# Optimization experiments

Hardware: AMD Instinct MI355X
Metric: run time of the kernel (lower is better)

The kernel has to match this reference:

```python
import math
import jax, jax.numpy as jnp
import numpy as np

N_NODES = 10000
N_EDGES = 160000
F_IN = 256
HID = 500
N_OUT = 100


def setup_inputs() -> dict:
    key = jax.random.key(0)
    ks = jax.random.split(key, 20)
    inp = {}
    inp['x'] = jax.random.normal(ks[0], (N_NODES, F_IN), jnp.float32)
    inp['edge_src'] = jax.random.randint(ks[1], (N_EDGES,), 0, N_NODES, jnp.int32)
    inp['edge_dst'] = jax.random.randint(ks[2], (N_EDGES,), 0, N_NODES, jnp.int32)
    inp['edge_weight'] = jax.random.uniform(ks[3], (N_EDGES,), jnp.float32)
    s1 = 1.0 / math.sqrt(F_IN)
    s2 = 1.0 / math.sqrt(HID)
    inp['W1_rel'] = jax.random.uniform(ks[4], (HID, F_IN), jnp.float32, -s1, s1)
    inp['b1'] = jax.random.uniform(ks[5], (HID,), jnp.float32, -s1, s1)
    inp['W1_root'] = jax.random.uniform(ks[6], (HID, F_IN), jnp.float32, -s1, s1)
    inp['p1_w'] = jax.random.uniform(ks[7], (HID,), jnp.float32, -s2, s2)
    inp['W2_rel'] = jax.random.uniform(ks[8], (HID, HID), jnp.float32, -s2, s2)
    inp['b2'] = jax.random.uniform(ks[9], (HID,), jnp.float32, -s2, s2)
    inp['W2_root'] = jax.random.uniform(ks[10], (HID, HID), jnp.float32, -s2, s2)
    inp['p2_w'] = jax.random.uniform(ks[11], (HID,), jnp.float32, -s2, s2)
    s3 = 1.0 / math.sqrt(1000)
    inp['lin1_W'] = jax.random.uniform(ks[12], (2000, 1000), jnp.float32, -s3, s3)
    inp['lin1_b'] = jax.random.uniform(ks[13], (2000,), jnp.float32, -s3, s3)
    s4 = 1.0 / math.sqrt(2000)
    inp['lin2_W'] = jax.random.uniform(ks[14], (4000, 2000), jnp.float32, -s4, s4)
    inp['lin2_b'] = jax.random.uniform(ks[15], (4000,), jnp.float32, -s4, s4)
    s5 = 1.0 / math.sqrt(4000)
    inp['lin3_W'] = jax.random.uniform(ks[16], (N_OUT, 4000), jnp.float32, -s5, s5)
    inp['lin3_b'] = jax.random.uniform(ks[17], (N_OUT,), jnp.float32, -s5, s5)
    return inp


def graph_conv(x, src, dst, w, W_rel, b_rel, W_root):
    # PyG GraphConv: out_i = W_rel @ sum_{j->i} w_ji * x_j + b + W_root @ x_i
    msg = x[src] * w[:, None]                              # [E, F]
    agg = jax.ops.segment_sum(msg, dst, num_segments=x.shape[0])
    return agg @ W_rel.T + b_rel + x @ W_root.T


def topk_pool(x, src, dst, w, p_w, ratio=0.5):
    # PyG TopKPooling: score = tanh(x @ p / ||p||); keep top-k; scale x by score.
    N = x.shape[0]
    k = int(math.ceil(ratio * N))
    score = jnp.tanh((x @ p_w) / jnp.linalg.norm(p_w))
    vals, perm = jax.lax.top_k(score, k)
    x_new = x[perm] * vals[:, None]
    # keep fixed-size edge list; dropped edges get weight 0 and point to node 0
    new_idx = jnp.zeros((N,), jnp.int32).at[perm].set(jnp.arange(k, dtype=jnp.int32))
    mask = jnp.zeros((N,), bool).at[perm].set(True)
    keep = mask[src] & mask[dst]
    src_new = jnp.where(keep, new_idx[src], 0)
    dst_new = jnp.where(keep, new_idx[dst], 0)
    w_new = jnp.where(keep, w, 0.0)
    return x_new, src_new, dst_new, w_new


def readout(x):
    # global max pool + global mean pool over the single graph -> [1, 2F]
    return jnp.concatenate([jnp.max(x, 0, keepdims=True), jnp.mean(x, 0, keepdims=True)], axis=1)


def reference(x, edge_src, edge_dst, edge_weight,
              W1_rel, b1, W1_root, p1_w,
              W2_rel, b2, W2_root, p2_w,
              lin1_W, lin1_b, lin2_W, lin2_b, lin3_W, lin3_b):
    h = jax.nn.relu(graph_conv(x, edge_src, edge_dst, edge_weight, W1_rel, b1, W1_root))
    h, s1, d1, w1 = topk_pool(h, edge_src, edge_dst, edge_weight, p1_w)
    x1 = readout(h)
    h = jax.nn.relu(graph_conv(h, s1, d1, w1, W2_rel, b2, W2_root))
    h, _, _, _ = topk_pool(h, s1, d1, w1, p2_w)
    x2 = readout(h)
    z = x1 + x2                                            # [1, 1000]
    z = jax.nn.relu(z @ lin1_W.T + lin1_b)
    z = jax.nn.relu(z @ lin2_W.T + lin2_b)                 # dropout is identity at eval
    return jax.nn.sigmoid(z @ lin3_W.T + lin3_b)
```

## Files before the change

kernel.cpp:

```cpp
#include <hip/hip_runtime.h>
#include <hip/hip_bf16.h>
#include <math.h>

#define NN1   10000
#define NE    160000
#define FIN   256
#define HID   500
#define K1    5000
#define NN2   5000
#define K2    2500

#define CSR_OFFS   0u
#define CSR_POS    10008u
#define CSR_EDGE   20008u
#define OFF_AGG    340016u
#define OFF_H      2900016u
#define OFF_XP2    (OFF_H + 2500000u)
#define OFF_XP1    7900016u
#define OFF_SC1    10400016u
#define OFF_RK1    10410016u
#define OFF_SC2    10420016u
#define OFF_RO     10430016u
#define OFF_Z      10432016u
#define OFF_T1     10433016u
#define OFF_T2     10435016u
#define OFF_INV    10439016u
#define OFF_CNT    10439024u
#define OFF_PM     10639024u
#define OFF_PS     10671024u
#define OFF_XB     10703024u
#define OFF_W1RB   11983024u
#define OFF_W1TB   12047024u
#define OFF_W2RB   12111024u
#define OFF_W2TB   12236024u
#define OFF_XP1B   12361024u
#define WS_FLOATS  13611024u

#define RCHUNK 500
#define ROSLAB1 64
#define ROSLAB2 32
#define RORPB   79

__device__ inline unsigned f2ord(float f) {
    unsigned u = __float_as_uint(f);
    return (u & 0x80000000u) ? ~u : (u | 0x80000000u);
}
__device__ inline unsigned long long rkey(float s, int j) {
    return ((unsigned long long)f2ord(s) << 32) | (unsigned)(0xFFFFFFFFu - (unsigned)j);
}
__device__ inline unsigned short bf16rn(float f) {
    unsigned u = __float_as_uint(f);
    u += 0x7FFFu + ((u >> 16) & 1u);
    return (unsigned short)(u >> 16);
}
__device__ inline float bf2f(unsigned short u) {
    return __uint_as_float((unsigned)u << 16);
}

typedef __attribute__((ext_vector_type(8))) short short8;
typedef __attribute__((ext_vector_type(4))) float floatx4;


__global__ __launch_bounds__(256) void k_prep(
    const float* __restrict__ x, unsigned short* __restrict__ xb,
    const float* __restrict__ w1r, unsigned short* __restrict__ w1rb,
    const float* __restrict__ w1t, unsigned short* __restrict__ w1tb,
    const float* __restrict__ w2r, unsigned short* __restrict__ w2rb,
    const float* __restrict__ w2t, unsigned short* __restrict__ w2tb,
    const float* __restrict__ p1, const float* __restrict__ p2,
    float* __restrict__ invn,
    const int* __restrict__ edst, int* __restrict__ pos) {
    __shared__ float red[256];
    int y = blockIdx.y;
    if (y < 5) {
        const float* s; unsigned short* d; int n;
        switch (y) {
            case 0: s = x;   d = xb;   n = NN1 * FIN; break;
            case 1: s = w1r; d = w1rb; n = HID * FIN; break;
            case 2: s = w1t; d = w1tb; n = HID * FIN; break;
            case 3: s = w2r; d = w2rb; n = HID * HID; break;
            default: s = w2t; d = w2tb; n = HID * HID; break;
        }
        int i = (blockIdx.x * 256 + threadIdx.x) * 4;
        if (i >= n) return;
        if (i + 3 < n) {
            float4 v = *(const float4*)(s + i);
            ushort4 o;
            o.x = bf16rn(v.x); o.y = bf16rn(v.y); o.z = bf16rn(v.z); o.w = bf16rn(v.w);
            *(ushort4*)(d + i) = o;
        } else {
            for (int q = 0; q < 4 && i + q < n; ++q) d[i + q] = bf16rn(s[i + q]);
        }
    } else if (y == 5) {
        if (blockIdx.x >= 2) return;
        const float* p = blockIdx.x ? p2 : p1;
        float s = 0.f;
        for (int i = threadIdx.x; i < HID; i += 256) { float v = p[i]; s += v * v; }
        red[threadIdx.x] = s; __syncthreads();
        for (int w = 128; w > 0; w >>= 1) {
            if (threadIdx.x < w) red[threadIdx.x] += red[threadIdx.x + w];
            __syncthreads();
        }
        if (threadIdx.x == 0) invn[blockIdx.x] = 1.0f / sqrtf(red[0]);
    } else {
        int e = blockIdx.x * 256 + threadIdx.x;
        if (e < NE) atomicAdd(&pos[edst[e]], 1);
    }
}

__global__ __launch_bounds__(1024) void k_scan(int* __restrict__ pos, int* __restrict__ offs) {
    __shared__ int tot[1024];
    int t = threadIdx.x;
    int base = t * 10;
    int loc[10]; int s = 0;
    #pragma unroll
    for (int q = 0; q < 10; ++q) {
        int v = (base + q < NN1) ? pos[base + q] : 0;
        loc[q] = s; s += v;
    }
    tot[t] = s; __syncthreads();
    for (int d = 1; d < 1024; d <<= 1) {
        int v = (t >= d) ? tot[t - d] : 0;
        __syncthreads();
        tot[t] += v;
        __syncthreads();
    }
    int excl = (t == 0) ? 0 : tot[t - 1];
    #pragma unroll
    for (int q = 0; q < 10; ++q)
        if (base + q < NN1) { int o = excl + loc[q]; offs[base + q] = o; pos[base + q] = o; }
    if (t == 1023) offs[NN1] = tot[1023];
}

__global__ void k_fill(const int* __restrict__ src, const int* __restrict__ dst,
                       const float* __restrict__ w, int* __restrict__ pos,
                       int2* __restrict__ ce) {
    int e = blockIdx.x * 256 + threadIdx.x;
    if (e >= NE) return;
    int slot = atomicAdd(&pos[dst[e]], 1);
    ce[slot] = make_int2(src[e], __float_as_int(w[e]));
}

__global__ __launch_bounds__(256) void k_gather1(
    const unsigned short* __restrict__ xb, const int* __restrict__ offs,
    const int2* __restrict__ ce, unsigned short* __restrict__ aggb) {
    int wave = (blockIdx.x * 256 + threadIdx.x) >> 6;
    int lane = threadIdx.x & 63;
    if (wave >= NN1) return;
    int b = offs[wave], e = offs[wave + 1];
    float4 acc = make_float4(0.f, 0.f, 0.f, 0.f);
    int2 nxt = (b < e) ? ce[b] : make_int2(0, 0);
    for (int p = b; p < e; ++p) {
        int2 cur = nxt;
        if (p + 1 < e) nxt = ce[p + 1];
        float we = __int_as_float(cur.y);
        ushort4 u = *(const ushort4*)(xb + (size_t)cur.x * FIN + lane * 4);
        acc.x += bf2f(u.x) * we; acc.y += bf2f(u.y) * we;
        acc.z += bf2f(u.z) * we; acc.w += bf2f(u.w) * we;
    }
    ushort4 o;
    o.x = bf16rn(acc.x); o.y = bf16rn(acc.y); o.z = bf16rn(acc.z); o.w = bf16rn(acc.w);
    *(ushort4*)(aggb + (size_t)wave * FIN + lane * 4) = o;
}

__global__ __launch_bounds__(256) void k_gather2(
    const unsigned short* __restrict__ Xb, const int* __restrict__ offs,
    const int2* __restrict__ ce, const int* __restrict__ rank,
    unsigned short* __restrict__ aggb) {
    int wave = (blockIdx.x * 256 + threadIdx.x) >> 6;
    int lane = threadIdx.x & 63;
    if (wave >= NN1) return;
    int rd = rank[wave];
    if (rd < 0) return;
    int b = offs[wave], e = offs[wave + 1];
    int c1 = 256 + lane * 4;
    float a0 = 0.f, a1 = 0.f, a2 = 0.f, a3 = 0.f;
    float b0 = 0.f, b1v = 0.f, b2 = 0.f, b3 = 0.f;
    int2 nxt = (b < e) ? ce[b] : make_int2(0, 0);
    for (int p = b; p < e; ++p) {
        int2 cur = nxt;
        if (p + 1 < e) nxt = ce[p + 1];
        int rs = rank[cur.x];
        if (rs < 0) continue;
        float we = __int_as_float(cur.y);
        const unsigned short* row = Xb + (size_t)rs * HID;
        ushort4 u = *(const ushort4*)(row + lane * 4);
        a0 += bf2f(u.x) * we; a1 += bf2f(u.y) * we;
        a2 += bf2f(u.z) * we; a3 += bf2f(u.w) * we;
        if (c1 < HID) {
            ushort4 u2 = *(const ushort4*)(row + c1);
            b0 += bf2f(u2.x) * we; b1v += bf2f(u2.y) * we;
            b2 += bf2f(u2.z) * we; b3 += bf2f(u2.w) * we;
        }
    }
    unsigned short* o = aggb + (size_t)rd * HID;
    ushort4 o1; o1.x = bf16rn(a0); o1.y = bf16rn(a1); o1.z = bf16rn(a2); o1.w = bf16rn(a3);
    *(ushort4*)(o + lane * 4) = o1;
    if (c1 < HID) {
        ushort4 o2; o2.x = bf16rn(b0); o2.y = bf16rn(b1v); o2.z = bf16rn(b2); o2.w = bf16rn(b3);
        *(ushort4*)(o + c1) = o2;
    }
}

__device__ inline short8 ld8g(const unsigned short* p, int gk, int K) {
    if (gk + 7 < K) return *(const short8*)p;
    unsigned short tmp[8] = {0,0,0,0,0,0,0,0};
    for (int q = 0; q < 8; ++q) if (gk + q < K) tmp[q] = p[q];
    return *(short8*)tmp;
}

#define GBK 64
#define APAD 72
__global__ __launch_bounds__(256) void k_gemm_bf16(
    const unsigned short* __restrict__ A1, const unsigned short* __restrict__ B1,
    const unsigned short* __restrict__ A2, const unsigned short* __restrict__ B2,
    const float* __restrict__ bias, unsigned short* __restrict__ C,
    int M, int N, int Ka, int Kb, int nbyRow) {
    int b = blockIdx.x;
    int xcd = b & 7, seq = b >> 3;
    int colT = seq & 7;
    int rowT = xcd + 8 * (seq >> 3);
    if (rowT >= nbyRow) return;
    int row0 = rowT * 64, col0 = colT * 64;

    __shared__ unsigned short As[64 * APAD];
    __shared__ unsigned short Bs[64 * APAD];
    int tid = threadIdx.x;
    int lane = tid & 63, wid = tid >> 6;
    int waveM = wid & 1, waveN = wid >> 1;
    int quad = lane >> 4, mrow = lane & 15;
    floatx4 acc[2][2] = {};

    int sr = tid >> 2;
    int sk = (tid & 3) * 16;

    int nka = (Ka + GBK - 1) / GBK;
    int nkb = (Kb + GBK - 1) / GBK;
    int niter = nka + nkb;

    short8 z8 = {0,0,0,0,0,0,0,0};
    short8 paA = z8, paB = z8, pbA = z8, pbB = z8;

    auto fetch = [&](const unsigned short* A, const unsigned short* B, int K, int k0) {
        int gr = row0 + sr, gn = col0 + sr, gk = k0 + sk;
        paA = z8; paB = z8; pbA = z8; pbB = z8;
        if (gr < M) {
            const unsigned short* p = A + (size_t)gr * K + gk;
            paA = ld8g(p, gk, K); paB = ld8g(p + 8, gk + 8, K);
        }
        if (gn < N) {
            const unsigned short* p = B + (size_t)gn * K + gk;
            pbA = ld8g(p, gk, K); pbB = ld8g(p + 8, gk + 8, K);
        }
    };

    fetch(A1, B1, Ka, 0);

    for (int it = 0; it < niter; ++it) {
        *(short8*)&As[sr * APAD + sk]     = paA;
        *(short8*)&As[sr * APAD + sk + 8] = paB;
        *(short8*)&Bs[sr * APAD + sk]     = pbA;
        *(short8*)&Bs[sr * APAD + sk + 8] = pbB;
        __syncthreads();
        if (it + 1 < niter) {
            int t = it + 1;
            int ph = (t >= nka);
            fetch(ph ? A2 : A1, ph ? B2 : B1, ph ? Kb : Ka, (ph ? t - nka : t) * GBK);
        }
        #pragma unroll
        for (int half = 0; half < 2; ++half) {
            int ko = half * 32 + quad * 8;
            short8 bfr[2];
            #pragma unroll
            for (int nt = 0; nt < 2; ++nt)
                bfr[nt] = *(short8*)&Bs[(waveN * 32 + nt * 16 + mrow) * APAD + ko];
            #pragma unroll
            for (int mt = 0; mt < 2; ++mt) {
                short8 afr = *(short8*)&As[(waveM * 32 + mt * 16 + mrow) * APAD + ko];
                #pragma unroll
                for (int nt = 0; nt < 2; ++nt)
                    acc[mt][nt] = __builtin_amdgcn_mfma_f32_16x16x32_bf16(
                        afr, bfr[nt], acc[mt][nt], 0, 0, 0);
            }
        }
        __syncthreads();
    }
    #pragma unroll
    for (int nt = 0; nt < 2; ++nt) {
        int col = col0 + waveN * 32 + nt * 16 + mrow;
        if (col >= N) continue;
        float bv = bias[col];
        #pragma unroll
        for (int mt = 0; mt < 2; ++mt) {
            int rbase = row0 + waveM * 32 + mt * 16 + quad * 4;
            #pragma unroll
            for (int r = 0; r < 4; ++r) {
                int row = rbase + r;
                if (row < M) C[(size_t)row * N + col] = bf16rn(fmaxf(acc[mt][nt][r] + bv, 0.f));
            }
        }
    }
}

__global__ __launch_bounds__(256) void k_scores(
    const unsigned short* __restrict__ Hb, const float* __restrict__ p,
    const float* __restrict__ invnorm, float* __restrict__ score, int Nn) {
    int wave = (blockIdx.x * 256 + threadIdx.x) >> 6;
    int lane = threadIdx.x & 63;
    if (wave >= Nn) return;
    const unsigned short* h = Hb + (size_t)wave * HID;
    float s = 0.f;
    for (int i = lane; i < HID; i += 64) s += bf2f(h[i]) * p[i];
    for (int off = 32; off > 0; off >>= 1) s += __shfl_down(s, off, 64);
    if (lane == 0) score[wave] = tanhf(s * invnorm[0]);
}

__global__ __launch_bounds__(256) void k_rank_partial(
    const float* __restrict__ score, int* __restrict__ cntp, int Nn) {
    __shared__ unsigned long long kj[RCHUNK];
    int j0 = blockIdx.y * RCHUNK;
    int jn = min(Nn - j0, RCHUNK);
    for (int t = threadIdx.x; t < jn; t += 256)
        kj[t] = rkey(score[j0 + t], j0 + t);
    __syncthreads();
    int i = blockIdx.x * 256 + threadIdx.x;
    if (i >= Nn) return;
    unsigned long long ki = rkey(score[i], i);
    int c = 0;
    #pragma unroll 4
    for (int q = 0; q < jn; ++q)
        c += (kj[q] > ki) ? 1 : 0;
    cntp[(size_t)blockIdx.y * Nn + i] = c;
}

__global__ __launch_bounds__(128) void k_gather_pool(
    const unsigned short* __restrict__ Hb, const float* __restrict__ score,
    const int* __restrict__ cntp, int Nn, int nchunk, int kk,
    int* __restrict__ rank_out, unsigned short* __restrict__ Xb) {
    __shared__ int csum[128];
    __shared__ int rsh;
    int i = blockIdx.x;
    int c = 0;
    for (int q = threadIdx.x; q < nchunk; q += 128) c += cntp[(size_t)q * Nn + i];
    csum[threadIdx.x] = c;
    __syncthreads();
    if (threadIdx.x == 0) {
        int t = 0;
        int lim = (nchunk < 128) ? nchunk : 128;
        for (int q = 0; q < lim; ++q) t += csum[q];
        int r = (t < kk) ? t : -1;
        if (rank_out) rank_out[i] = r;
        rsh = r;
    }
    __syncthreads();
    int r = rsh;
    if (r < 0) return;
    float sc = score[i];
    int cc = threadIdx.x;
    if (cc < HID / 4) {
        ushort4 u = *(const ushort4*)(Hb + (size_t)i * HID + cc * 4);
        ushort4 o;
        o.x = bf16rn(bf2f(u.x) * sc); o.y = bf16rn(bf2f(u.y) * sc);
        o.z = bf16rn(bf2f(u.z) * sc); o.w = bf16rn(bf2f(u.w) * sc);
        *(ushort4*)(Xb + (size_t)r * HID + cc * 4) = o;
    }
}

__global__ __launch_bounds__(256) void k_readout_slab(
    const unsigned short* __restrict__ X, int rows, int rpb,
    float* __restrict__ pmax, float* __restrict__ psum) {
    __shared__ float4 lmx[4][64];
    __shared__ float4 lsm[4][64];
    int lane = threadIdx.x & 63;
    int rgrp = threadIdx.x >> 6;
    int c4 = blockIdx.x * 64 + lane;
    int r0 = blockIdx.y * rpb;
    int r1 = min(rows, r0 + rpb);
    float4 mx = make_float4(-INFINITY, -INFINITY, -INFINITY, -INFINITY);
    float4 sm = make_float4(0.f, 0.f, 0.f, 0.f);
    if (c4 < HID / 4) {
        for (int r = r0 + rgrp; r < r1; r += 4) {
            ushort4 u = *(const ushort4*)(X + (size_t)r * HID + c4 * 4);
            float vx = bf2f(u.x), vy = bf2f(u.y), vz = bf2f(u.z), vw = bf2f(u.w);
            mx.x = fmaxf(mx.x, vx); mx.y = fmaxf(mx.y, vy);
            mx.z = fmaxf(mx.z, vz); mx.w = fmaxf(mx.w, vw);
            sm.x += vx; sm.y += vy; sm.z += vz; sm.w += vw;
        }
    }
    lmx[rgrp][lane] = mx; lsm[rgrp][lane] = sm;
    __syncthreads();
    if (rgrp == 0 && c4 < HID / 4) {
        #pragma unroll
        for (int g = 1; g < 4; ++g) {
            float4 m2 = lmx[g][lane], s2 = lsm[g][lane];
            mx.x = fmaxf(mx.x, m2.x); mx.y = fmaxf(mx.y, m2.y);
            mx.z = fmaxf(mx.z, m2.z); mx.w = fmaxf(mx.w, m2.w);
            sm.x += s2.x; sm.y += s2.y; sm.z += s2.z; sm.w += s2.w;
        }
        *(float4*)(pmax + (size_t)blockIdx.y * HID + c4 * 4) = mx;
        *(float4*)(psum + (size_t)blockIdx.y * HID + c4 * 4) = sm;
    }
}

__global__ __launch_bounds__(64) void k_ro_final(
    const float* __restrict__ pmax, const float* __restrict__ psum, int nslab,
    float* __restrict__ fmax, float* __restrict__ fsum) {
    int j = blockIdx.x * 64 + threadIdx.x;
    if (j >= HID) return;
    float mx = -INFINITY, sm = 0.f;
    for (int s = 0; s < nslab; ++s) {
        mx = fmaxf(mx, pmax[(size_t)s * HID + j]);
        sm += psum[(size_t)s * HID + j];
    }
    fmax[j] = mx; fsum[j] = sm;
}

__global__ __launch_bounds__(64) void k_ro2_combine(
    const float* __restrict__ pmax, const float* __restrict__ psum, int nslab,
    const float* __restrict__ max1, const float* __restrict__ sum1,
    float* __restrict__ z) {
    int j = blockIdx.x * 64 + threadIdx.x;
    if (j >= HID) return;
    float mx = -INFINITY, sm = 0.f;
    for (int s = 0; s < nslab; ++s) {
        mx = fmaxf(mx, pmax[(size_t)s * HID + j]);
        sm += psum[(size_t)s * HID + j];
    }
    z[j] = max1[j] + mx;
    z[HID + j] = sum1[j] * (1.0f / (float)K1) + sm * (1.0f / (float)K2);
}

__global__ __launch_bounds__(256) void k_mv(
    const float* __restrict__ v, const float* __restrict__ W,
    const float* __restrict__ bias, float* __restrict__ y,
    int rowsN, int K, int act) {
    int wave = (blockIdx.x * 256 + threadIdx.x) >> 6;
    int lane = threadIdx.x & 63;
    if (wave >= rowsN) return;
    const float* wr = W + (size_t)wave * K;
    float s = 0.f;
    for (int c = lane * 4; c < K; c += 256) {
        float4 a = *(const float4*)(wr + c);
        float4 xv = *(const float4*)(v + c);
        s += a.x * xv.x + a.y * xv.y + a.z * xv.z + a.w * xv.w;
    }
    for (int off = 32; off > 0; off >>= 1) s += __shfl_down(s, off, 64);
    if (lane == 0) {
        float r = s + bias[wave];
        y[wave] = (act == 0) ? fmaxf(r, 0.f) : 1.f / (1.f + expf(-r));
    }
}

extern "C" void kernel_launch(void* const* d_in, const int* in_sizes, int n_in,
                              void* d_out, int out_size, void* d_ws, size_t ws_size,
                              hipStream_t stream) {
    const float* x      = (const float*)d_in[0];
    const int*   esrc   = (const int*)d_in[1];
    const int*   edst   = (const int*)d_in[2];
    const float* ew     = (const float*)d_in[3];
    const float* W1_rel = (const float*)d_in[4];
    const float* b1     = (const float*)d_in[5];
    const float* W1_root= (const float*)d_in[6];
    const float* p1     = (const float*)d_in[7];
    const float* W2_rel = (const float*)d_in[8];
    const float* b2     = (const float*)d_in[9];
    const float* W2_root= (const float*)d_in[10];
    const float* p2     = (const float*)d_in[11];
    const float* l1W    = (const float*)d_in[12];
    const float* l1b    = (const float*)d_in[13];
    const float* l2W    = (const float*)d_in[14];
    const float* l2b    = (const float*)d_in[15];
    const float* l3W    = (const float*)d_in[16];
    const float* l3b    = (const float*)d_in[17];
    float* out = (float*)d_out;
    float* ws  = (float*)d_ws;

    if (ws_size < (size_t)WS_FLOATS * sizeof(float)) return;

    int*            offs  = (int*)(ws + CSR_OFFS);
    int*            pos   = (int*)(ws + CSR_POS);
    int2*           ce    = (int2*)(ws + CSR_EDGE);
    unsigned short* aggb  = (unsigned short*)(ws + OFF_AGG);
    unsigned short* hb    = (unsigned short*)(ws + OFF_H);
    unsigned short* xp2b  = (unsigned short*)(ws + OFF_XP2);
    float*          sc1   = ws + OFF_SC1;
    int*            rk1   = (int*)(ws + OFF_RK1);
    float*          sc2   = ws + OFF_SC2;
    float*          max1  = ws + OFF_RO;
    float*          sum1  = ws + OFF_RO + 500;
    float*          zbuf  = ws + OFF_Z;
    float*          t1    = ws + OFF_T1;
    float*          t2    = ws + OFF_T2;
    float*          invn  = ws + OFF_INV;
    int*            cntp  = (int*)(ws + OFF_CNT);
    float*          pmax  = ws + OFF_PM;
    float*          psum  = ws + OFF_PS;
    unsigned short* xb    = (unsigned short*)(ws + OFF_XB);
    unsigned short* w1rb  = (unsigned short*)(ws + OFF_W1RB);
    unsigned short* w1tb  = (unsigned short*)(ws + OFF_W1TB);
    unsigned short* w2rb  = (unsigned short*)(ws + OFF_W2RB);
    unsigned short* w2tb  = (unsigned short*)(ws + OFF_W2TB);
    unsigned short* xp1b  = (unsigned short*)(ws + OFF_XP1B);

    hipMemsetAsync(pos, 0, NN1 * sizeof(int), stream);
    k_prep<<<dim3(2500, 7), 256, 0, stream>>>(
        x, xb, W1_rel, w1rb, W1_root, w1tb, W2_rel, w2rb, W2_root, w2tb,
        p1, p2, invn, edst, pos);
    k_scan<<<1, 1024, 0, stream>>>(pos, offs);
    k_fill<<<(NE + 255) / 256, 256, 0, stream>>>(esrc, edst, ew, pos, ce);

    k_gather1<<<(NN1 * 64 + 255) / 256, 256, 0, stream>>>(xb, offs, ce, aggb);
    {
        int nby = (NN1 + 63) / 64;
        int nblk = 64 * ((nby + 7) / 8);
        k_gemm_bf16<<<nblk, 256, 0, stream>>>(
            aggb, w1rb, xb, w1tb, b1, hb, NN1, HID, FIN, FIN, nby);
    }

    k_scores<<<(NN1 * 64 + 255) / 256, 256, 0, stream>>>(hb, p1, invn + 0, sc1, NN1);
    k_rank_partial<<<dim3((NN1 + 255) / 256, NN1 / RCHUNK), 256, 0, stream>>>(sc1, cntp, NN1);
    k_gather_pool<<<NN1, 128, 0, stream>>>(hb, sc1, cntp, NN1, NN1 / RCHUNK, K1, rk1, xp1b);
    k_readout_slab<<<dim3(2, ROSLAB1), 256, 0, stream>>>(xp1b, K1, RORPB, pmax, psum);
    k_ro_final<<<(HID + 63) / 64, 64, 0, stream>>>(pmax, psum, ROSLAB1, max1, sum1);

    k_gather2<<<(NN1 * 64 + 255) / 256, 256, 0, stream>>>(xp1b, offs, ce, rk1, aggb);
    {
        int nby = (NN2 + 63) / 64;
        int nblk = 64 * ((nby + 7) / 8);
        k_gemm_bf16<<<nblk, 256, 0, stream>>>(
            aggb, w2rb, xp1b, w2tb, b2, hb, NN2, HID, HID, HID, nby);
    }

    k_scores<<<(NN2 * 64 + 255) / 256, 256, 0, stream>>>(hb, p2, invn + 1, sc2, NN2);
    k_rank_partial<<<dim3((NN2 + 255) / 256, NN2 / RCHUNK), 256, 0, stream>>>(sc2, cntp, NN2);
    k_gather_pool<<<NN2, 128, 0, stream>>>(hb, sc2, cntp, NN2, NN2 / RCHUNK, K2,
                                           (int*)nullptr, xp2b);
    k_readout_slab<<<dim3(2, ROSLAB2), 256, 0, stream>>>(xp2b, K2, RORPB, pmax, psum);
    k_ro2_combine<<<(HID + 63) / 64, 64, 0, stream>>>(pmax, psum, ROSLAB2, max1, sum1, zbuf);

    k_mv<<<(2000 * 64) / 256, 256, 0, stream>>>(zbuf, l1W, l1b, t1, 2000, 1000, 0);
    k_mv<<<(4000 * 64) / 256, 256, 0, stream>>>(t1, l2W, l2b, t2, 4000, 2000, 0);
    k_mv<<<(100 * 64) / 256, 256, 0, stream>>>(t2, l3W, l3b, out, 100, 4000, 1);
}
```

Baseline: 341.4 us.

## Fuse TopK score dot-product into GEMM epilogue and merge readout combine kernels

The GEMM epilogue now computes per-row partial dot products of the ReLU output with the pooling vector, writing 16 column-tile partials per row. The rank and gather-pool kernels sum these partials, so the separate score kernel that re-read the bf16 hidden matrix is removed, and tanh is applied in gather-pool. The two readout-finalize kernels are merged into one combine kernel using separate partial buffers. The intent is to cut a full pass over the hidden activations and two launches. In exchange the rank kernel re-sums 16 partials for every key, and scores now come from fp32 values before bf16 rounding, which can change tie ordering slightly.

```diff
diff --git a/kernel.cpp b/kernel.cpp
--- a/kernel.cpp
+++ b/kernel.cpp
@@ -16,25 +16,24 @@
 #define OFF_AGG    340016u
 #define OFF_H      2900016u
 #define OFF_XP2    (OFF_H + 2500000u)
-#define OFF_XP1    7900016u
-#define OFF_SC1    10400016u
+#define OFF_SCP    7900016u
 #define OFF_RK1    10410016u
-#define OFF_SC2    10420016u
-#define OFF_RO     10430016u
 #define OFF_Z      10432016u
 #define OFF_T1     10433016u
 #define OFF_T2     10435016u
 #define OFF_INV    10439016u
 #define OFF_CNT    10439024u
-#define OFF_PM     10639024u
-#define OFF_PS     10671024u
+#define OFF_PM1    10639024u
+#define OFF_PS1    10671024u
 #define OFF_XB     10703024u
 #define OFF_W1RB   11983024u
 #define OFF_W1TB   12047024u
 #define OFF_W2RB   12111024u
 #define OFF_W2TB   12236024u
 #define OFF_XP1B   12361024u
-#define WS_FLOATS  13611024u
+#define OFF_PM2    13611024u
+#define OFF_PS2    13627024u
+#define WS_FLOATS  13643024u
 
 #define RCHUNK 500
 #define ROSLAB1 64
@@ -214,7 +213,8 @@
 __global__ __launch_bounds__(256) void k_gemm_bf16(
     const unsigned short* __restrict__ A1, const unsigned short* __restrict__ B1,
     const unsigned short* __restrict__ A2, const unsigned short* __restrict__ B2,
-    const float* __restrict__ bias, unsigned short* __restrict__ C,
+    const float* __restrict__ bias, const float* __restrict__ pv,
+    unsigned short* __restrict__ C, float* __restrict__ scpart,
     int M, int N, int Ka, int Kb, int nbyRow) {
     int b = blockIdx.x;
     int xcd = b & 7, seq = b >> 3;
@@ -285,47 +285,58 @@
         }
         __syncthreads();
     }
+    float ps[2][4] = {};
     #pragma unroll
     for (int nt = 0; nt < 2; ++nt) {
         int col = col0 + waveN * 32 + nt * 16 + mrow;
         if (col >= N) continue;
         float bv = bias[col];
+        float pc = pv[col];
         #pragma unroll
         for (int mt = 0; mt < 2; ++mt) {
             int rbase = row0 + waveM * 32 + mt * 16 + quad * 4;
             #pragma unroll
             for (int r = 0; r < 4; ++r) {
+                float v = fmaxf(acc[mt][nt][r] + bv, 0.f);
                 int row = rbase + r;
-                if (row < M) C[(size_t)row * N + col] = bf16rn(fmaxf(acc[mt][nt][r] + bv, 0.f));
+                if (row < M) C[(size_t)row * N + col] = bf16rn(v);
+                ps[mt][r] += v * pc;
             }
         }
     }
-}
-
-__global__ __launch_bounds__(256) void k_scores(
-    const unsigned short* __restrict__ Hb, const float* __restrict__ p,
-    const float* __restrict__ invnorm, float* __restrict__ score, int Nn) {
-    int wave = (blockIdx.x * 256 + threadIdx.x) >> 6;
-    int lane = threadIdx.x & 63;
-    if (wave >= Nn) return;
-    const unsigned short* h = Hb + (size_t)wave * HID;
-    float s = 0.f;
-    for (int i = lane; i < HID; i += 64) s += bf2f(h[i]) * p[i];
-    for (int off = 32; off > 0; off >>= 1) s += __shfl_down(s, off, 64);
-    if (lane == 0) score[wave] = tanhf(s * invnorm[0]);
+    int part = colT * 2 + waveN;
+    #pragma unroll
+    for (int mt = 0; mt < 2; ++mt)
+        #pragma unroll
+        for (int r = 0; r < 4; ++r) {
+            float v = ps[mt][r];
+            v += __shfl_xor(v, 1, 64); v += __shfl_xor(v, 2, 64);
+            v += __shfl_xor(v, 4, 64); v += __shfl_xor(v, 8, 64);
+            if (mrow == 0) {
+                int row = row0 + waveM * 32 + mt * 16 + quad * 4 + r;
+                if (row < M) scpart[(size_t)part * M + row] = v;
+            }
+        }
 }
 
 __global__ __launch_bounds__(256) void k_rank_partial(
-    const float* __restrict__ score, int* __restrict__ cntp, int Nn) {
+    const float* __restrict__ scpart, int* __restrict__ cntp, int Nn) {
     __shared__ unsigned long long kj[RCHUNK];
     int j0 = blockIdx.y * RCHUNK;
     int jn = min(Nn - j0, RCHUNK);
-    for (int t = threadIdx.x; t < jn; t += 256)
-        kj[t] = rkey(score[j0 + t], j0 + t);
+    for (int t = threadIdx.x; t < jn; t += 256) {
+        float s = 0.f;
+        #pragma unroll
+        for (int q = 0; q < 16; ++q) s += scpart[(size_t)q * Nn + j0 + t];
+        kj[t] = rkey(s, j0 + t);
+    }
     __syncthreads();
     int i = blockIdx.x * 256 + threadIdx.x;
     if (i >= Nn) return;
-    unsigned long long ki = rkey(score[i], i);
+    float si = 0.f;
+    #pragma unroll
+    for (int q = 0; q < 16; ++q) si += scpart[(size_t)q * Nn + i];
+    unsigned long long ki = rkey(si, i);
     int c = 0;
     #pragma unroll 4
     for (int q = 0; q < jn; ++q)
@@ -334,28 +345,35 @@
 }
 
 __global__ __launch_bounds__(128) void k_gather_pool(
-    const unsigned short* __restrict__ Hb, const float* __restrict__ score,
+    const unsigned short* __restrict__ Hb, const float* __restrict__ scpart,
+    const float* __restrict__ invn,
     const int* __restrict__ cntp, int Nn, int nchunk, int kk,
     int* __restrict__ rank_out, unsigned short* __restrict__ Xb) {
     __shared__ int csum[128];
+    __shared__ float ssum[128];
     __shared__ int rsh;
+    __shared__ float scsh;
     int i = blockIdx.x;
     int c = 0;
     for (int q = threadIdx.x; q < nchunk; q += 128) c += cntp[(size_t)q * Nn + i];
-    csum[threadIdx.x] = c;
+    float s = (threadIdx.x < 16) ? scpart[(size_t)threadIdx.x * Nn + i] : 0.f;
+    csum[threadIdx.x] = c; ssum[threadIdx.x] = s;
     __syncthreads();
     if (threadIdx.x == 0) {
         int t = 0;
         int lim = (nchunk < 128) ? nchunk : 128;
         for (int q = 0; q < lim; ++q) t += csum[q];
+        float st = 0.f;
+        for (int q = 0; q < 16; ++q) st += ssum[q];
         int r = (t < kk) ? t : -1;
         if (rank_out) rank_out[i] = r;
         rsh = r;
+        scsh = tanhf(st * invn[0]);
     }
     __syncthreads();
     int r = rsh;
     if (r < 0) return;
-    float sc = score[i];
+    float sc = scsh;
     int cc = threadIdx.x;
     if (cc < HID / 4) {
         ushort4 u = *(const ushort4*)(Hb + (size_t)i * HID + cc * 4);
@@ -402,32 +420,24 @@
     }
 }
 
-__global__ __launch_bounds__(64) void k_ro_final(
-    const float* __restrict__ pmax, const float* __restrict__ psum, int nslab,
-    float* __restrict__ fmax, float* __restrict__ fsum) {
-    int j = blockIdx.x * 64 + threadIdx.x;
-    if (j >= HID) return;
-    float mx = -INFINITY, sm = 0.f;
-    for (int s = 0; s < nslab; ++s) {
-        mx = fmaxf(mx, pmax[(size_t)s * HID + j]);
-        sm += psum[(size_t)s * HID + j];
-    }
-    fmax[j] = mx; fsum[j] = sm;
-}
-
-__global__ __launch_bounds__(64) void k_ro2_combine(
-    const float* __restrict__ pmax, const float* __restrict__ psum, int nslab,
-    const float* __restrict__ max1, const float* __restrict__ sum1,
+__global__ __launch_bounds__(64) void k_combine_all(
+    const float* __restrict__ pm1, const float* __restrict__ ps1, int ns1,
+    const float* __restrict__ pm2, const float* __restrict__ ps2, int ns2,
     float* __restrict__ z) {
     int j = blockIdx.x * 64 + threadIdx.x;
     if (j >= HID) return;
-    float mx = -INFINITY, sm = 0.f;
-    for (int s = 0; s < nslab; ++s) {
-        mx = fmaxf(mx, pmax[(size_t)s * HID + j]);
-        sm += psum[(size_t)s * HID + j];
-    }
-    z[j] = max1[j] + mx;
-    z[HID + j] = sum1[j] * (1.0f / (float)K1) + sm * (1.0f / (float)K2);
+    float m1 = -INFINITY, s1 = 0.f;
+    for (int s = 0; s < ns1; ++s) {
+        m1 = fmaxf(m1, pm1[(size_t)s * HID + j]);
+        s1 += ps1[(size_t)s * HID + j];
+    }
+    float m2 = -INFINITY, s2 = 0.f;
+    for (int s = 0; s < ns2; ++s) {
+        m2 = fmaxf(m2, pm2[(size_t)s * HID + j]);
+        s2 += ps2[(size_t)s * HID + j];
+    }
+    z[j] = m1 + m2;
+    z[HID + j] = s1 * (1.0f / (float)K1) + s2 * (1.0f / (float)K2);
 }
 
 __global__ __launch_bounds__(256) void k_mv(
@@ -483,18 +493,17 @@
     unsigned short* aggb  = (unsigned short*)(ws + OFF_AGG);
     unsigned short* hb    = (unsigned short*)(ws + OFF_H);
     unsigned short* xp2b  = (unsigned short*)(ws + OFF_XP2);
-    float*          sc1   = ws + OFF_SC1;
+    float*          scp   = ws + OFF_SCP;
     int*            rk1   = (int*)(ws + OFF_RK1);
-    float*          sc2   = ws + OFF_SC2;
-    float*          max1  = ws + OFF_RO;
-    float*          sum1  = ws + OFF_RO + 500;
     float*          zbuf  = ws + OFF_Z;
     float*          t1    = ws + OFF_T1;
     float*          t2    = ws + OFF_T2;
     float*          invn  = ws + OFF_INV;
     int*            cntp  = (int*)(ws + OFF_CNT);
-    float*          pmax  = ws + OFF_PM;
-    float*          psum  = ws + OFF_PS;
+    float*          pm1   = ws + OFF_PM1;
+    float*          ps1   = ws + OFF_PS1;
+    float*          pm2   = ws + OFF_PM2;
+    float*          ps2   = ws + OFF_PS2;
     unsigned short* xb    = (unsigned short*)(ws + OFF_XB);
     unsigned short* w1rb  = (unsigned short*)(ws + OFF_W1RB);
     unsigned short* w1tb  = (unsigned short*)(ws + OFF_W1TB);
@@ -514,29 +523,27 @@
         int nby = (NN1 + 63) / 64;
         int nblk = 64 * ((nby + 7) / 8);
         k_gemm_bf16<<<nblk, 256, 0, stream>>>(
-            aggb, w1rb, xb, w1tb, b1, hb, NN1, HID, FIN, FIN, nby);
-    }
-
-    k_scores<<<(NN1 * 64 + 255) / 256, 256, 0, stream>>>(hb, p1, invn + 0, sc1, NN1);
-    k_rank_partial<<<dim3((NN1 + 255) / 256, NN1 / RCHUNK), 256, 0, stream>>>(sc1, cntp, NN1);
-    k_gather_pool<<<NN1, 128, 0, stream>>>(hb, sc1, cntp, NN1, NN1 / RCHUNK, K1, rk1, xp1b);
-    k_readout_slab<<<dim3(2, ROSLAB1), 256, 0, stream>>>(xp1b, K1, RORPB, pmax, psum);
-    k_ro_final<<<(HID + 63) / 64, 64, 0, stream>>>(pmax, psum, ROSLAB1, max1, sum1);
+            aggb, w1rb, xb, w1tb, b1, p1, hb, scp, NN1, HID, FIN, FIN, nby);
+    }
+
+    k_rank_partial<<<dim3((NN1 + 255) / 256, NN1 / RCHUNK), 256, 0, stream>>>(scp, cntp, NN1);
+    k_gather_pool<<<NN1, 128, 0, stream>>>(hb, scp, invn + 0, cntp, NN1, NN1 / RCHUNK, K1,
+                                           rk1, xp1b);
+    k_readout_slab<<<dim3(2, ROSLAB1), 256, 0, stream>>>(xp1b, K1, RORPB, pm1, ps1);
 
     k_gather2<<<(NN1 * 64 + 255) / 256, 256, 0, stream>>>(xp1b, offs, ce, rk1, aggb);
     {
         int nby = (NN2 + 63) / 64;
         int nblk = 64 * ((nby + 7) / 8);
         k_gemm_bf16<<<nblk, 256, 0, stream>>>(
-            aggb, w2rb, xp1b, w2tb, b2, hb, NN2, HID, HID, HID, nby);
-    }
-
-    k_scores<<<(NN2 * 64 + 255) / 256, 256, 0, stream>>>(hb, p2, invn + 1, sc2, NN2);
-    k_rank_partial<<<dim3((NN2 + 255) / 256, NN2 / RCHUNK), 256, 0, stream>>>(sc2, cntp, NN2);
-    k_gather_pool<<<NN2, 128, 0, stream>>>(hb, sc2, cntp, NN2, NN2 / RCHUNK, K2,
+            aggb, w2rb, xp1b, w2tb, b2, p2, hb, scp, NN2, HID, HID, HID, nby);
+    }
+
+    k_rank_partial<<<dim3((NN2 + 255) / 256, NN2 / RCHUNK), 256, 0, stream>>>(scp, cntp, NN2);
+    k_gather_pool<<<NN2, 128, 0, stream>>>(hb, scp, invn + 1, cntp, NN2, NN2 / RCHUNK, K2,
                                            (int*)nullptr, xp2b);
-    k_readout_slab<<<dim3(2, ROSLAB2), 256, 0, stream>>>(xp2b, K2, RORPB, pmax, psum);
-    k_ro2_combine<<<(HID + 63) / 64, 64, 0, stream>>>(pmax, psum, ROSLAB2, max1, sum1, zbuf);
+    k_readout_slab<<<dim3(2, ROSLAB2), 256, 0, stream>>>(xp2b, K2, RORPB, pm2, ps2);
+    k_combine_all<<<(HID + 63) / 64, 64, 0, stream>>>(pm1, ps1, ROSLAB1, pm2, ps2, ROSLAB2, zbuf);
 
     k_mv<<<(2000 * 64) / 256, 256, 0, stream>>>(zbuf, l1W, l1b, t1, 2000, 1000, 0);
     k_mv<<<(4000 * 64) / 256, 256, 0, stream>>>(t1, l2W, l2b, t2, 4000, 2000, 0);
```

Result: faster. 329.1 us (-3.6%).
